# Kernel tuning notes

Measured on AMD Instinct MI355X. Metric: run time of the kernel, lower is better.

Reference implementation:

```python
import jax, jax.numpy as jnp
import numpy as np

NUM_HEADS = 12
SCALE = 1.0 / np.sqrt(768 // NUM_HEADS)  # 0.125


def setup_inputs() -> dict:
    key = jax.random.key(0)
    k1, k2, k3, k4, k5 = jax.random.split(key, 5)
    B, N, C = 4, 2048, 768
    x = jax.random.normal(k1, (B, N, C), dtype=jnp.float32)
    qkv_w = jax.random.normal(k2, (3 * C, C), dtype=jnp.float32) * 0.02
    qkv_b = jax.random.normal(k3, (3 * C,), dtype=jnp.float32) * 0.02
    proj_w = jax.random.normal(k4, (C, C), dtype=jnp.float32) * 0.02
    proj_b = jax.random.normal(k5, (C,), dtype=jnp.float32) * 0.02
    return {"x": x, "qkv_w": qkv_w, "qkv_b": qkv_b, "proj_w": proj_w, "proj_b": proj_b}


def reference(x, qkv_w, qkv_b, proj_w, proj_b):
    B, N, C = x.shape
    H = NUM_HEADS
    Dh = C // H
    # qkv projection (torch Linear: x @ W^T + b)
    qkv = x @ qkv_w.T + qkv_b                      # [B, N, 3C]
    qkv = qkv.reshape(B, N, 3, H, Dh).transpose(2, 0, 3, 1, 4)  # [3, B, H, N, Dh]
    q, k, v = qkv[0], qkv[1], qkv[2]
    q = q * SCALE
    attn = jnp.einsum("bhnd,bhmd->bhnm", q, k)     # [B, H, N, N]
    attn = jax.nn.softmax(attn, axis=-1)
    out = jnp.einsum("bhnm,bhmd->bhnd", attn, v)   # [B, H, N, Dh]
    out = out.transpose(0, 2, 1, 3).reshape(B, N, C)
    out = out @ proj_w.T + proj_b
    return out
```

## Files before the change

### kernel.cpp

```cpp
#include <hip/hip_runtime.h>
#include <math.h>

typedef __attribute__((ext_vector_type(8))) short short8;
typedef __attribute__((ext_vector_type(4))) float f32x4;
typedef __attribute__((ext_vector_type(16))) float f32x16;

namespace {

constexpr int B  = 4;
constexpr int N  = 2048;
constexpr int C  = 768;
constexpr int H  = 12;
constexpr int Dh = 64;
constexpr int M  = B * N;
constexpr int C3 = 3 * C;

constexpr float QSCALE = 0.125f * 1.4426950408889634f;

__device__ inline unsigned short f2bf(float x) {
  unsigned int u = __float_as_uint(x);
  return (unsigned short)((u + 0x7fffu + ((u >> 16) & 1u)) >> 16);
}

__device__ inline unsigned cvt_pk_bf16(float lo, float hi) {
  unsigned r;
  asm("v_cvt_pk_bf16_f32 %0, %1, %2" : "=v"(r) : "v"(lo), "v"(hi));
  return r;
}

__device__ inline void gload_lds16(const void* g, void* lds) {
  __builtin_amdgcn_global_load_lds(
      (const __attribute__((address_space(1))) void*)g,
      (__attribute__((address_space(3))) void*)lds, 16, 0, 0);
}

__device__ inline float max3f(float a, float b, float c) {
  return fmaxf(fmaxf(a, b), c);
}

__global__ __launch_bounds__(256) void cvt_all3(
    const float* __restrict__ x, const float* __restrict__ qw,
    const float* __restrict__ pw, unsigned short* __restrict__ xbf,
    unsigned short* __restrict__ wqkv, unsigned short* __restrict__ wproj) {
  constexpr int n1 = M * C / 4, n2 = C3 * C / 4, n3 = C * C / 4;
  constexpr int tot = n1 + n2 + n3;
  for (int i = blockIdx.x * 256 + threadIdx.x; i < tot; i += gridDim.x * 256) {
    const float4* s; unsigned short* d; int j;
    if (i < n1)            { s = (const float4*)x;  d = xbf;   j = i; }
    else if (i < n1 + n2)  { s = (const float4*)qw; d = wqkv;  j = i - n1; }
    else                   { s = (const float4*)pw; d = wproj; j = i - n1 - n2; }
    float4 v = s[j];
    ushort4 o;
    o.x = f2bf(v.x); o.y = f2bf(v.y); o.z = f2bf(v.z); o.w = f2bf(v.w);
    reinterpret_cast<ushort4*>(d)[j] = o;
  }
}

template <bool QKV_EPI>
__global__ __launch_bounds__(256, 2) void gemm_mfma_bt(
    const unsigned short* __restrict__ A, const unsigned short* __restrict__ Bw,
    const float* __restrict__ bias, void* __restrict__ outp, int Nd, int K) {
  __shared__ alignas(16) unsigned short lA[128 * 64];
  __shared__ alignas(16) unsigned short lB[128 * 64];
  const int t = threadIdx.x, wave = t >> 6, lane = t & 63;
  const int bm = blockIdx.x * 128, bn = blockIdx.y * 128;
  const int wr = (wave >> 1) * 64, wc = (wave & 1) * 64;

  f32x4 acc[4][4];
#pragma unroll
  for (int i = 0; i < 4; ++i)
#pragma unroll
    for (int j = 0; j < 4; ++j) acc[i][j] = (f32x4){0.f, 0.f, 0.f, 0.f};

  const int srow = lane >> 3;
  const int scol = ((lane & 7) ^ srow) * 8;
  const int rb0  = wave * 32;

  for (int k0 = 0; k0 < K; k0 += 64) {
#pragma unroll
    for (int i = 0; i < 4; ++i) {
      const int rb = rb0 + i * 8;
      const unsigned short* ga = A  + (size_t)(bm + rb + srow) * K + k0 + scol;
      const unsigned short* gb = Bw + (size_t)(bn + rb + srow) * K + k0 + scol;
      gload_lds16(ga, (char*)lA + rb * 128);
      gload_lds16(gb, (char*)lB + rb * 128);
    }
    __syncthreads();

#pragma unroll
    for (int kc = 0; kc < 2; ++kc) {
      short8 af[4], bfr[4];
#pragma unroll
      for (int mt = 0; mt < 4; ++mt) {
        const int row = wr + mt * 16 + (lane & 15);
        const int q = (row * 128 + kc * 64 + (lane >> 4) * 16) ^ ((row & 7) << 4);
        af[mt] = *reinterpret_cast<const short8*>((const char*)lA + q);
      }
#pragma unroll
      for (int nt = 0; nt < 4; ++nt) {
        const int row = wc + nt * 16 + (lane & 15);
        const int q = (row * 128 + kc * 64 + (lane >> 4) * 16) ^ ((row & 7) << 4);
        bfr[nt] = *reinterpret_cast<const short8*>((const char*)lB + q);
      }
#pragma unroll
      for (int mt = 0; mt < 4; ++mt)
#pragma unroll
        for (int nt = 0; nt < 4; ++nt)
          acc[mt][nt] = __builtin_amdgcn_mfma_f32_16x16x32_bf16(
              af[mt], bfr[nt], acc[mt][nt], 0, 0, 0);
    }
    __syncthreads();
  }

  const int r0 = (lane >> 4) * 4;
  const int cl = lane & 15;
#pragma unroll
  for (int nt = 0; nt < 4; ++nt) {
    const int col = bn + wc + nt * 16 + cl;
    const float bs = bias[col];
    const float sc = (QKV_EPI && col < C) ? QSCALE : 1.0f;
#pragma unroll
    for (int mt = 0; mt < 4; ++mt) {
#pragma unroll
      for (int r = 0; r < 4; ++r) {
        const size_t row = bm + wr + mt * 16 + r0 + r;
        const float v = acc[mt][nt][r] + bs;
        if (QKV_EPI)
          ((unsigned short*)outp)[row * Nd + col] = f2bf(v * sc);
        else
          ((float*)outp)[row * Nd + col] = v;
      }
    }
  }
}

__global__ __launch_bounds__(256) void vt_prepass(
    const unsigned short* __restrict__ qkvbf, unsigned short* __restrict__ vt) {
  const int bh = blockIdx.x, b = bh / H, h = bh % H;
  const int nt = blockIdx.y;
  __shared__ unsigned short tile[64][72];
  const int t = threadIdx.x;
  const int r = t >> 2, ch = (t & 3) * 16;

  const unsigned short* src =
      qkvbf + (size_t)(b * N + nt * 64 + r) * C3 + 2 * C + h * Dh + ch;
  *reinterpret_cast<int4*>(&tile[r][ch])     = *reinterpret_cast<const int4*>(src);
  *reinterpret_cast<int4*>(&tile[r][ch + 8]) = *reinterpret_cast<const int4*>(src + 8);
  __syncthreads();

  alignas(16) unsigned short vals[16];
#pragma unroll
  for (int i = 0; i < 16; ++i) vals[i] = tile[ch + i][r];
  unsigned short* dst = vt + ((size_t)bh * Dh + r) * N + nt * 64 + ch;
  *reinterpret_cast<int4*>(dst)     = *reinterpret_cast<int4*>(&vals[0]);
  *reinterpret_cast<int4*>(dst + 8) = *reinterpret_cast<int4*>(&vals[8]);
}

__global__ __launch_bounds__(128, 2) void attn_mfma32(
    const unsigned short* __restrict__ qkvbf,
    const unsigned short* __restrict__ vt,
    unsigned short* __restrict__ ctx) {
  const int bh = blockIdx.x, b = bh / H, h = bh % H;
  const int qt = blockIdx.y;
  const int t = threadIdx.x;
  const int wave = t >> 6, lane = t & 63;
  const int ql = lane & 31;
  const int hi = lane >> 5;
  const int q0 = qt * 128 + wave * 64;

  __shared__ alignas(16) char lds[2][16384];

  short8 qfa[4], qfb[4];
  {
    const unsigned short* qa =
        qkvbf + (size_t)(b * N + q0 + ql) * C3 + h * Dh + 8 * hi;
    const unsigned short* qb = qa + (size_t)32 * C3;
#pragma unroll
    for (int s = 0; s < 4; ++s) {
      int4 va = *reinterpret_cast<const int4*>(qa + 16 * s);
      int4 vb = *reinterpret_cast<const int4*>(qb + 16 * s);
      qfa[s] = *reinterpret_cast<short8*>(&va);
      qfb[s] = *reinterpret_cast<short8*>(&vb);
    }
  }

  f32x16 zz;
#pragma unroll
  for (int r = 0; r < 16; ++r) zz[r] = 0.f;
  f32x16 oa0 = zz, oa1 = zz, ob0 = zz, ob1 = zz;
  float mra = -INFINITY, mrb = -INFINITY, la = 0.f, lb = 0.f;

  const int rl = lane >> 3;
  const int cse = ((lane & 7) ^ rl) * 8;
  const unsigned short* kstg =
      qkvbf + (size_t)(b * N + rl) * C3 + C + h * Dh + cse;
  const unsigned short* vstg = vt + ((size_t)bh * Dh + rl) * N + cse;

  auto stage = [&](int kt, char* buf) {
    if (wave == 0) {
      const unsigned short* kp = kstg + (size_t)(kt * 64) * C3;
#pragma unroll
      for (int j = 0; j < 8; ++j)
        gload_lds16(kp + (size_t)(j * 8) * C3, buf + j * 1024);
    } else {
      const unsigned short* vp = vstg + kt * 64;
#pragma unroll
      for (int j = 0; j < 8; ++j)
        gload_lds16(vp + (size_t)(j * 8) * N, buf + 8192 + j * 1024);
    }
  };

  constexpr int NT = N / 64;

  auto kaddr = [&](int row, int s) {
    return (row * 128 + 32 * s + 16 * hi) ^ ((row & 7) << 4);
  };

  stage(0, lds[0]);
  __syncthreads();

  for (int kt = 0; kt < NT; ++kt) {
    const char* bufc = lds[kt & 1];
    if (kt + 1 < NT) stage(kt + 1, lds[(kt + 1) & 1]);

    short8 k0[4], k1[4];
#pragma unroll
    for (int s = 0; s < 4; ++s) {
      k0[s] = *reinterpret_cast<const short8*>(bufc + kaddr(ql, s));
      k1[s] = *reinterpret_cast<const short8*>(bufc + kaddr(32 + ql, s));
    }

    f32x16 sa0, sa1, sb0, sb1;
    __builtin_amdgcn_s_setprio(1);
    sa0 = __builtin_amdgcn_mfma_f32_32x32x16_bf16(k0[0], qfa[0], zz, 0, 0, 0);
    sa1 = __builtin_amdgcn_mfma_f32_32x32x16_bf16(k1[0], qfa[0], zz, 0, 0, 0);
    sb0 = __builtin_amdgcn_mfma_f32_32x32x16_bf16(k0[0], qfb[0], zz, 0, 0, 0);
    sb1 = __builtin_amdgcn_mfma_f32_32x32x16_bf16(k1[0], qfb[0], zz, 0, 0, 0);
#pragma unroll
    for (int s = 1; s < 4; ++s) {
      sa0 = __builtin_amdgcn_mfma_f32_32x32x16_bf16(k0[s], qfa[s], sa0, 0, 0, 0);
      sa1 = __builtin_amdgcn_mfma_f32_32x32x16_bf16(k1[s], qfa[s], sa1, 0, 0, 0);
      sb0 = __builtin_amdgcn_mfma_f32_32x32x16_bf16(k0[s], qfb[s], sb0, 0, 0, 0);
      sb1 = __builtin_amdgcn_mfma_f32_32x32x16_bf16(k1[s], qfb[s], sb1, 0, 0, 0);
    }
    __builtin_amdgcn_s_setprio(0);

    short8 vfr[8];
    const char* bufv = bufc + 8192;
#pragma unroll
    for (int s = 0; s < 4; ++s) {
      vfr[2 * s]     = *reinterpret_cast<const short8*>(bufv + kaddr(ql, s));
      vfr[2 * s + 1] = *reinterpret_cast<const short8*>(bufv + kaddr(32 + ql, s));
    }

    auto rmax = [&](const f32x16& x, const f32x16& y) {
      float t0 = max3f(x[0], x[1], x[2]);
      float t1 = max3f(x[3], x[4], x[5]);
      float t2 = max3f(x[6], x[7], x[8]);
      float t3 = max3f(x[9], x[10], x[11]);
      float t4 = max3f(x[12], x[13], x[14]);
      float t5 = max3f(x[15], y[0], y[1]);
      float t6 = max3f(y[2], y[3], y[4]);
      float t7 = max3f(y[5], y[6], y[7]);
      float t8 = max3f(y[8], y[9], y[10]);
      float t9 = max3f(y[11], y[12], y[13]);
      float ta = fmaxf(y[14], y[15]);
      t0 = max3f(t0, t1, t2);
      t3 = max3f(t3, t4, t5);
      t6 = max3f(t6, t7, t8);
      t9 = max3f(t9, ta, t0);
      return max3f(t3, t6, t9);
    };
    const float mxa = rmax(sa0, sa1);
    const float mxb = rmax(sb0, sb1);
    const bool fast = (mxa <= mra + 8.f) && (mxb <= mrb + 8.f);
    if (!__all(fast)) {
      const float nma = fmaxf(mra, fmaxf(mxa, __shfl_xor(mxa, 32)));
      const float nmb = fmaxf(mrb, fmaxf(mxb, __shfl_xor(mxb, 32)));
      const float ca = __builtin_amdgcn_exp2f(mra - nma);
      const float cb = __builtin_amdgcn_exp2f(mrb - nmb);
      la *= ca; lb *= cb;
#pragma unroll
      for (int r = 0; r < 16; ++r) {
        const int qr = (r & 3) + 8 * (r >> 2) + 4 * hi;
        const float cra = __shfl(ca, qr);
        const float crb = __shfl(cb, qr);
        oa0[r] *= cra; oa1[r] *= cra;
        ob0[r] *= crb; ob1[r] *= crb;
      }
      mra = nma; mrb = nmb;
    }

    auto mkfrag = [&](const f32x16& sh, float mr, float& lacc,
                      short8& fA, short8& fB) {
      float e[16];
#pragma unroll
      for (int r = 0; r < 16; ++r) e[r] = __builtin_amdgcn_exp2f(sh[r] - mr);
      lacc += (((e[0] + e[1]) + (e[2] + e[3])) + ((e[4] + e[5]) + (e[6] + e[7]))) +
              (((e[8] + e[9]) + (e[10] + e[11])) + ((e[12] + e[13]) + (e[14] + e[15])));
      unsigned w[8];
#pragma unroll
      for (int tt = 0; tt < 4; ++tt) {
        w[2 * tt]     = cvt_pk_bf16(e[4 * tt], e[4 * tt + 1]);
        w[2 * tt + 1] = cvt_pk_bf16(e[4 * tt + 2], e[4 * tt + 3]);
      }
      unsigned a0 = w[0], a1 = w[1], b0 = w[2], b1 = w[3];
      asm("v_permlane32_swap_b32 %0, %1" : "+v"(a0), "+v"(b0));
      asm("v_permlane32_swap_b32 %0, %1" : "+v"(a1), "+v"(b1));
      int4 p0; p0.x = a0; p0.y = a1; p0.z = b0; p0.w = b1;
      fA = *reinterpret_cast<short8*>(&p0);
      unsigned c0 = w[4], c1 = w[5], d0 = w[6], d1 = w[7];
      asm("v_permlane32_swap_b32 %0, %1" : "+v"(c0), "+v"(d0));
      asm("v_permlane32_swap_b32 %0, %1" : "+v"(c1), "+v"(d1));
      int4 p1; p1.x = c0; p1.y = c1; p1.z = d0; p1.w = d1;
      fB = *reinterpret_cast<short8*>(&p1);
    };
    short8 pa0, pa1, pa2, pa3, pb0, pb1, pb2, pb3;
    mkfrag(sa0, mra, la, pa0, pa1);
    mkfrag(sa1, mra, la, pa2, pa3);
    mkfrag(sb0, mrb, lb, pb0, pb1);
    mkfrag(sb1, mrb, lb, pb2, pb3);

    __builtin_amdgcn_s_setprio(1);
    oa0 = __builtin_amdgcn_mfma_f32_32x32x16_bf16(pa0, vfr[0], oa0, 0, 0, 0);
    oa1 = __builtin_amdgcn_mfma_f32_32x32x16_bf16(pa0, vfr[1], oa1, 0, 0, 0);
    ob0 = __builtin_amdgcn_mfma_f32_32x32x16_bf16(pb0, vfr[0], ob0, 0, 0, 0);
    ob1 = __builtin_amdgcn_mfma_f32_32x32x16_bf16(pb0, vfr[1], ob1, 0, 0, 0);
    oa0 = __builtin_amdgcn_mfma_f32_32x32x16_bf16(pa1, vfr[2], oa0, 0, 0, 0);
    oa1 = __builtin_amdgcn_mfma_f32_32x32x16_bf16(pa1, vfr[3], oa1, 0, 0, 0);
    ob0 = __builtin_amdgcn_mfma_f32_32x32x16_bf16(pb1, vfr[2], ob0, 0, 0, 0);
    ob1 = __builtin_amdgcn_mfma_f32_32x32x16_bf16(pb1, vfr[3], ob1, 0, 0, 0);
    oa0 = __builtin_amdgcn_mfma_f32_32x32x16_bf16(pa2, vfr[4], oa0, 0, 0, 0);
    oa1 = __builtin_amdgcn_mfma_f32_32x32x16_bf16(pa2, vfr[5], oa1, 0, 0, 0);
    ob0 = __builtin_amdgcn_mfma_f32_32x32x16_bf16(pb2, vfr[4], ob0, 0, 0, 0);
    ob1 = __builtin_amdgcn_mfma_f32_32x32x16_bf16(pb2, vfr[5], ob1, 0, 0, 0);
    oa0 = __builtin_amdgcn_mfma_f32_32x32x16_bf16(pa3, vfr[6], oa0, 0, 0, 0);
    oa1 = __builtin_amdgcn_mfma_f32_32x32x16_bf16(pa3, vfr[7], oa1, 0, 0, 0);
    ob0 = __builtin_amdgcn_mfma_f32_32x32x16_bf16(pb3, vfr[6], ob0, 0, 0, 0);
    ob1 = __builtin_amdgcn_mfma_f32_32x32x16_bf16(pb3, vfr[7], ob1, 0, 0, 0);
    __builtin_amdgcn_s_setprio(0);

    __syncthreads();
  }

  la += __shfl_xor(la, 32);
  lb += __shfl_xor(lb, 32);
  const float inva = 1.f / la;
  const float invb = 1.f / lb;
#pragma unroll
  for (int r = 0; r < 16; ++r) {
    const int qr = (r & 3) + 8 * (r >> 2) + 4 * hi;
    const float ira = __shfl(inva, qr);
    const float irb = __shfl(invb, qr);
    unsigned short* rowa = ctx + (size_t)(b * N + q0 + qr) * C + h * Dh;
    unsigned short* rowb = rowa + (size_t)32 * C;
    rowa[ql]      = f2bf(oa0[r] * ira);
    rowa[32 + ql] = f2bf(oa1[r] * ira);
    rowb[ql]      = f2bf(ob0[r] * irb);
    rowb[32 + ql] = f2bf(ob1[r] * irb);
  }
}

}

extern "C" void kernel_launch(void* const* d_in, const int* in_sizes, int n_in,
                              void* d_out, int out_size, void* d_ws, size_t ws_size,
                              hipStream_t stream) {
  const float* x      = (const float*)d_in[0];
  const float* qkv_w  = (const float*)d_in[1];
  const float* qkv_b  = (const float*)d_in[2];
  const float* proj_w = (const float*)d_in[3];
  const float* proj_b = (const float*)d_in[4];
  float* out = (float*)d_out;

  unsigned short* qkvbf = (unsigned short*)d_ws;
  unsigned short* ctx   = qkvbf + (size_t)M * C3;
  unsigned short* vt    = ctx + (size_t)M * C;
  unsigned short* xbf   = vt + (size_t)M * C;
  unsigned short* wqkv  = xbf + (size_t)M * C;
  unsigned short* wproj = wqkv + (size_t)C3 * C;

  cvt_all3<<<2048, 256, 0, stream>>>(x, qkv_w, proj_w, xbf, wqkv, wproj);

  gemm_mfma_bt<true>
      <<<dim3(M / 128, C3 / 128), 256, 0, stream>>>(xbf, wqkv, qkv_b, qkvbf, C3, C);
  vt_prepass<<<dim3(B * H, N / 64), 256, 0, stream>>>(qkvbf, vt);
  attn_mfma32<<<dim3(B * H, N / 128), 128, 0, stream>>>(qkvbf, vt, ctx);
  gemm_mfma_bt<false>
      <<<dim3(M / 128, C / 128), 256, 0, stream>>>(ctx, wproj, proj_b, out, C, C);
}
```

Measured before the change: 148.4 us.

## Split attention KV range in two and merge partial softmax results

Splits the flash-attention key/value loop into two halves run by separate blocks (grid z=2). Each block writes its unnormalized partial output in bf16 along with the running max and sum, and a new merge kernel combines them with log-sum-exp rescaling. The goal is to double the block count so more of the GPU's compute units are busy, since the original grid of 768 two-wave blocks may underfill the device. The cost is extra global traffic for the partials, an extra kernel launch, and some precision loss from storing unnormalized bf16 partials; part0 reuses the xbf buffer.

```diff
diff --git a/kernel.cpp b/kernel.cpp
--- a/kernel.cpp
+++ b/kernel.cpp
@@ -20,6 +20,10 @@
 __device__ inline unsigned short f2bf(float x) {
   unsigned int u = __float_as_uint(x);
   return (unsigned short)((u + 0x7fffu + ((u >> 16) & 1u)) >> 16);
+}
+
+__device__ inline float bf2f(unsigned short x) {
+  return __uint_as_float((unsigned)x << 16);
 }
 
 __device__ inline unsigned cvt_pk_bf16(float lo, float hi) {
@@ -159,9 +163,15 @@
 __global__ __launch_bounds__(128, 2) void attn_mfma32(
     const unsigned short* __restrict__ qkvbf,
     const unsigned short* __restrict__ vt,
-    unsigned short* __restrict__ ctx) {
+    unsigned short* __restrict__ part0, unsigned short* __restrict__ part1,
+    float2* __restrict__ ml0, float2* __restrict__ ml1) {
   const int bh = blockIdx.x, b = bh / H, h = bh % H;
   const int qt = blockIdx.y;
+  const int z  = blockIdx.z;
+  const int kv0 = z * (N / 2);
+  unsigned short* part = z ? part1 : part0;
+  float2* mlp = z ? ml1 : ml0;
+
   const int t = threadIdx.x;
   const int wave = t >> 6, lane = t & 63;
   const int ql = lane & 31;
@@ -193,8 +203,8 @@
   const int rl = lane >> 3;
   const int cse = ((lane & 7) ^ rl) * 8;
   const unsigned short* kstg =
-      qkvbf + (size_t)(b * N + rl) * C3 + C + h * Dh + cse;
-  const unsigned short* vstg = vt + ((size_t)bh * Dh + rl) * N + cse;
+      qkvbf + (size_t)(b * N + kv0 + rl) * C3 + C + h * Dh + cse;
+  const unsigned short* vstg = vt + ((size_t)bh * Dh + rl) * N + kv0 + cse;
 
   auto stage = [&](int kt, char* buf) {
     if (wave == 0) {
@@ -210,7 +220,7 @@
     }
   };
 
-  constexpr int NT = N / 64;
+  constexpr int NT = N / 2 / 64;
 
   auto kaddr = [&](int row, int s) {
     return (row * 128 + 32 * s + 16 * hi) ^ ((row & 7) << 4);
@@ -345,20 +355,52 @@
 
   la += __shfl_xor(la, 32);
   lb += __shfl_xor(lb, 32);
-  const float inva = 1.f / la;
-  const float invb = 1.f / lb;
+  if (hi == 0) {
+    mlp[(size_t)bh * N + q0 + ql]      = make_float2(mra, la);
+    mlp[(size_t)bh * N + q0 + 32 + ql] = make_float2(mrb, lb);
+  }
 #pragma unroll
   for (int r = 0; r < 16; ++r) {
     const int qr = (r & 3) + 8 * (r >> 2) + 4 * hi;
-    const float ira = __shfl(inva, qr);
-    const float irb = __shfl(invb, qr);
-    unsigned short* rowa = ctx + (size_t)(b * N + q0 + qr) * C + h * Dh;
+    unsigned short* rowa = part + (size_t)(b * N + q0 + qr) * C + h * Dh;
     unsigned short* rowb = rowa + (size_t)32 * C;
-    rowa[ql]      = f2bf(oa0[r] * ira);
-    rowa[32 + ql] = f2bf(oa1[r] * ira);
-    rowb[ql]      = f2bf(ob0[r] * irb);
-    rowb[32 + ql] = f2bf(ob1[r] * irb);
-  }
+    rowa[ql]      = f2bf(oa0[r]);
+    rowa[32 + ql] = f2bf(oa1[r]);
+    rowb[ql]      = f2bf(ob0[r]);
+    rowb[32 + ql] = f2bf(ob1[r]);
+  }
+}
+
+__global__ __launch_bounds__(256) void merge_splits(
+    const unsigned short* __restrict__ p0, const unsigned short* __restrict__ p1,
+    const float2* __restrict__ ml0, const float2* __restrict__ ml1,
+    unsigned short* __restrict__ ctx) {
+  const int idx = blockIdx.x * 256 + threadIdx.x;
+  const int r = idx / 96, c = (idx % 96) * 8;
+  const int b = r >> 11, n = r & 2047, h = c >> 6;
+  const size_t mli = (size_t)(b * H + h) * N + n;
+  const float2 u = ml0[mli], v = ml1[mli];
+  const float m  = fmaxf(u.x, v.x);
+  const float c0 = __builtin_amdgcn_exp2f(u.x - m);
+  const float c1 = __builtin_amdgcn_exp2f(v.x - m);
+  const float inv = 1.f / (u.y * c0 + v.y * c1);
+  const float s0 = c0 * inv, s1 = c1 * inv;
+  const size_t off = (size_t)r * C + c;
+  int4 a = *reinterpret_cast<const int4*>(p0 + off);
+  int4 bb = *reinterpret_cast<const int4*>(p1 + off);
+  short8 x0 = *reinterpret_cast<short8*>(&a);
+  short8 x1 = *reinterpret_cast<short8*>(&bb);
+  unsigned w[4];
+#pragma unroll
+  for (int j = 0; j < 4; ++j) {
+    float f0 = bf2f((unsigned short)x0[2 * j]) * s0 +
+               bf2f((unsigned short)x1[2 * j]) * s1;
+    float f1 = bf2f((unsigned short)x0[2 * j + 1]) * s0 +
+               bf2f((unsigned short)x1[2 * j + 1]) * s1;
+    w[j] = cvt_pk_bf16(f0, f1);
+  }
+  int4 o; o.x = w[0]; o.y = w[1]; o.z = w[2]; o.w = w[3];
+  *reinterpret_cast<int4*>(ctx + off) = o;
 }
 
 }
@@ -379,13 +421,19 @@
   unsigned short* xbf   = vt + (size_t)M * C;
   unsigned short* wqkv  = xbf + (size_t)M * C;
   unsigned short* wproj = wqkv + (size_t)C3 * C;
+  unsigned short* part1 = wproj + (size_t)C * C;
+  float2* ml0 = (float2*)(part1 + (size_t)M * C);
+  float2* ml1 = ml0 + (size_t)B * H * N;
+  unsigned short* part0 = xbf;
 
   cvt_all3<<<2048, 256, 0, stream>>>(x, qkv_w, proj_w, xbf, wqkv, wproj);
 
   gemm_mfma_bt<true>
       <<<dim3(M / 128, C3 / 128), 256, 0, stream>>>(xbf, wqkv, qkv_b, qkvbf, C3, C);
   vt_prepass<<<dim3(B * H, N / 64), 256, 0, stream>>>(qkvbf, vt);
-  attn_mfma32<<<dim3(B * H, N / 128), 128, 0, stream>>>(qkvbf, vt, ctx);
+  attn_mfma32<<<dim3(B * H, N / 128, 2), 128, 0, stream>>>(
+      qkvbf, vt, part0, part1, ml0, ml1);
+  merge_splits<<<M * 96 / 256, 256, 0, stream>>>(part0, part1, ml0, ml1, ctx);
   gemm_mfma_bt<false>
       <<<dim3(M / 128, C / 128), 256, 0, stream>>>(ctx, wproj, proj_b, out, C, C);
 }
```

Measured after the change: 159.6 us. 1.08x slower.

## Software-pipeline attention: overlap next QK^T with softmax and PV, triple-buffer LDS

Applied to the files above, without the earlier changes.

The attention kernel is restructured so the QK^T MFMAs for the next key tile are issued before the softmax and PV of the current tile, using two ping-ponged score register sets and a three-deep LDS ring with explicit vmcnt waits. The row-sum is now computed on the matrix cores by multiplying P with a ones fragment, which removes the VALU adds and the final cross-lane shuffles. The goal is to hide exp/VALU latency behind MFMA work and to cut barrier stalls. The costs are higher register pressure from the extra score and l accumulators, the dropped occupancy hint of 2 blocks, and 48KB of LDS per block.

```diff
diff --git a/kernel.cpp b/kernel.cpp
--- a/kernel.cpp
+++ b/kernel.cpp
@@ -36,6 +36,61 @@
 
 __device__ inline float max3f(float a, float b, float c) {
   return fmaxf(fmaxf(a, b), c);
+}
+
+__device__ __forceinline__ float rmax2(const f32x16& x, const f32x16& y) {
+  float t0 = max3f(x[0], x[1], x[2]);
+  float t1 = max3f(x[3], x[4], x[5]);
+  float t2 = max3f(x[6], x[7], x[8]);
+  float t3 = max3f(x[9], x[10], x[11]);
+  float t4 = max3f(x[12], x[13], x[14]);
+  float t5 = max3f(x[15], y[0], y[1]);
+  float t6 = max3f(y[2], y[3], y[4]);
+  float t7 = max3f(y[5], y[6], y[7]);
+  float t8 = max3f(y[8], y[9], y[10]);
+  float t9 = max3f(y[11], y[12], y[13]);
+  float ta = fmaxf(y[14], y[15]);
+  t0 = max3f(t0, t1, t2);
+  t3 = max3f(t3, t4, t5);
+  t6 = max3f(t6, t7, t8);
+  t9 = max3f(t9, ta, t0);
+  return max3f(t3, t6, t9);
+}
+
+__device__ __forceinline__ void mkfrag(const f32x16& sh, float mr,
+                                       short8& fA, short8& fB) {
+  float e[16];
+#pragma unroll
+  for (int r = 0; r < 16; ++r) e[r] = __builtin_amdgcn_exp2f(sh[r] - mr);
+  unsigned w[8];
+#pragma unroll
+  for (int tt = 0; tt < 4; ++tt) {
+    w[2 * tt]     = cvt_pk_bf16(e[4 * tt], e[4 * tt + 1]);
+    w[2 * tt + 1] = cvt_pk_bf16(e[4 * tt + 2], e[4 * tt + 3]);
+  }
+  unsigned a0 = w[0], a1 = w[1], b0 = w[2], b1 = w[3];
+  asm("v_permlane32_swap_b32 %0, %1" : "+v"(a0), "+v"(b0));
+  asm("v_permlane32_swap_b32 %0, %1" : "+v"(a1), "+v"(b1));
+  int4 p0; p0.x = (int)a0; p0.y = (int)a1; p0.z = (int)b0; p0.w = (int)b1;
+  fA = *reinterpret_cast<short8*>(&p0);
+  unsigned c0 = w[4], c1 = w[5], d0 = w[6], d1 = w[7];
+  asm("v_permlane32_swap_b32 %0, %1" : "+v"(c0), "+v"(d0));
+  asm("v_permlane32_swap_b32 %0, %1" : "+v"(c1), "+v"(d1));
+  int4 p1; p1.x = (int)c0; p1.y = (int)c1; p1.z = (int)d0; p1.w = (int)d1;
+  fB = *reinterpret_cast<short8*>(&p1);
+}
+
+__device__ __forceinline__ void rescaleO(
+    f32x16& oa0, f32x16& oa1, f32x16& ob0, f32x16& ob1,
+    f32x16& la, f32x16& lb, float ca, float cb, int hi) {
+#pragma unroll
+  for (int r = 0; r < 16; ++r) {
+    const int qr = (r & 3) + 8 * (r >> 2) + 4 * hi;
+    const float cra = __shfl(ca, qr);
+    const float crb = __shfl(cb, qr);
+    oa0[r] *= cra; oa1[r] *= cra; la[r] *= cra;
+    ob0[r] *= crb; ob1[r] *= crb; lb[r] *= crb;
+  }
 }
 
 __global__ __launch_bounds__(256) void cvt_all3(
@@ -156,7 +211,92 @@
   *reinterpret_cast<int4*>(dst + 8) = *reinterpret_cast<int4*>(&vals[8]);
 }
 
-__global__ __launch_bounds__(128, 2) void attn_mfma32(
+#define QK_ACC4(SA0, SA1, SB0, SB1, K0, K1, S)                                 \
+  SA0 = __builtin_amdgcn_mfma_f32_32x32x16_bf16(K0, qfa[S], SA0, 0, 0, 0);     \
+  SA1 = __builtin_amdgcn_mfma_f32_32x32x16_bf16(K1, qfa[S], SA1, 0, 0, 0);     \
+  SB0 = __builtin_amdgcn_mfma_f32_32x32x16_bf16(K0, qfb[S], SB0, 0, 0, 0);     \
+  SB1 = __builtin_amdgcn_mfma_f32_32x32x16_bf16(K1, qfb[S], SB1, 0, 0, 0);
+
+#define ATTN_STEP(T, SA0C, SA1C, SB0C, SB1C, SA0N, SA1N, SB0N, SB1N)           \
+  {                                                                            \
+    const int T_ = (T);                                                        \
+    if (T_ + 1 < NT) {                                                         \
+      asm volatile("s_waitcnt vmcnt(0)" ::: "memory");                         \
+      __builtin_amdgcn_s_barrier();                                            \
+      if (T_ + 2 < NT) stage(T_ + 2);                                          \
+      const char* bn_ = lds[(T_ + 1) % 3];                                     \
+      short8 ka_ = *reinterpret_cast<const short8*>(bn_ + kaddr(ql, 0));       \
+      short8 kb_ = *reinterpret_cast<const short8*>(bn_ + kaddr(32 + ql, 0));  \
+      __builtin_amdgcn_s_setprio(1);                                           \
+      SA0N = __builtin_amdgcn_mfma_f32_32x32x16_bf16(ka_, qfa[0], zz, 0, 0, 0);\
+      SA1N = __builtin_amdgcn_mfma_f32_32x32x16_bf16(kb_, qfa[0], zz, 0, 0, 0);\
+      SB0N = __builtin_amdgcn_mfma_f32_32x32x16_bf16(ka_, qfb[0], zz, 0, 0, 0);\
+      SB1N = __builtin_amdgcn_mfma_f32_32x32x16_bf16(kb_, qfb[0], zz, 0, 0, 0);\
+      ka_ = *reinterpret_cast<const short8*>(bn_ + kaddr(ql, 1));              \
+      kb_ = *reinterpret_cast<const short8*>(bn_ + kaddr(32 + ql, 1));         \
+      QK_ACC4(SA0N, SA1N, SB0N, SB1N, ka_, kb_, 1)                             \
+      ka_ = *reinterpret_cast<const short8*>(bn_ + kaddr(ql, 2));              \
+      kb_ = *reinterpret_cast<const short8*>(bn_ + kaddr(32 + ql, 2));         \
+      QK_ACC4(SA0N, SA1N, SB0N, SB1N, ka_, kb_, 2)                             \
+      ka_ = *reinterpret_cast<const short8*>(bn_ + kaddr(ql, 3));              \
+      kb_ = *reinterpret_cast<const short8*>(bn_ + kaddr(32 + ql, 3));         \
+      QK_ACC4(SA0N, SA1N, SB0N, SB1N, ka_, kb_, 3)                             \
+      __builtin_amdgcn_s_setprio(0);                                           \
+    }                                                                          \
+    const char* bc_ = lds[T_ % 3];                                             \
+    const char* bv_ = bc_ + 8192;                                              \
+    short8 vf0_ = *reinterpret_cast<const short8*>(bv_ + kaddr(ql, 0));        \
+    short8 vf1_ = *reinterpret_cast<const short8*>(bv_ + kaddr(32 + ql, 0));   \
+    short8 vf2_ = *reinterpret_cast<const short8*>(bv_ + kaddr(ql, 1));        \
+    short8 vf3_ = *reinterpret_cast<const short8*>(bv_ + kaddr(32 + ql, 1));   \
+    short8 vf4_ = *reinterpret_cast<const short8*>(bv_ + kaddr(ql, 2));        \
+    short8 vf5_ = *reinterpret_cast<const short8*>(bv_ + kaddr(32 + ql, 2));   \
+    short8 vf6_ = *reinterpret_cast<const short8*>(bv_ + kaddr(ql, 3));        \
+    short8 vf7_ = *reinterpret_cast<const short8*>(bv_ + kaddr(32 + ql, 3));   \
+    const float mxa_ = rmax2(SA0C, SA1C);                                      \
+    const float mxb_ = rmax2(SB0C, SB1C);                                      \
+    if (!__all((mxa_ <= mra + 8.f) && (mxb_ <= mrb + 8.f))) {                  \
+      const float nma_ = fmaxf(mra, fmaxf(mxa_, __shfl_xor(mxa_, 32)));        \
+      const float nmb_ = fmaxf(mrb, fmaxf(mxb_, __shfl_xor(mxb_, 32)));        \
+      const float ca_ = __builtin_amdgcn_exp2f(mra - nma_);                    \
+      const float cb_ = __builtin_amdgcn_exp2f(mrb - nmb_);                    \
+      rescaleO(oa0, oa1, ob0, ob1, l_a, l_b, ca_, cb_, hi);                    \
+      mra = nma_; mrb = nmb_;                                                  \
+    }                                                                          \
+    short8 pa0_, pa1_, pa2_, pa3_, pb0_, pb1_, pb2_, pb3_;                     \
+    mkfrag(SA0C, mra, pa0_, pa1_);                                             \
+    mkfrag(SA1C, mra, pa2_, pa3_);                                             \
+    mkfrag(SB0C, mrb, pb0_, pb1_);                                             \
+    mkfrag(SB1C, mrb, pb2_, pb3_);                                             \
+    __builtin_amdgcn_s_setprio(1);                                             \
+    l_a = __builtin_amdgcn_mfma_f32_32x32x16_bf16(pa0_, ones, l_a, 0, 0, 0);   \
+    l_b = __builtin_amdgcn_mfma_f32_32x32x16_bf16(pb0_, ones, l_b, 0, 0, 0);   \
+    oa0 = __builtin_amdgcn_mfma_f32_32x32x16_bf16(pa0_, vf0_, oa0, 0, 0, 0);   \
+    oa1 = __builtin_amdgcn_mfma_f32_32x32x16_bf16(pa0_, vf1_, oa1, 0, 0, 0);   \
+    ob0 = __builtin_amdgcn_mfma_f32_32x32x16_bf16(pb0_, vf0_, ob0, 0, 0, 0);   \
+    ob1 = __builtin_amdgcn_mfma_f32_32x32x16_bf16(pb0_, vf1_, ob1, 0, 0, 0);   \
+    l_a = __builtin_amdgcn_mfma_f32_32x32x16_bf16(pa1_, ones, l_a, 0, 0, 0);   \
+    l_b = __builtin_amdgcn_mfma_f32_32x32x16_bf16(pb1_, ones, l_b, 0, 0, 0);   \
+    oa0 = __builtin_amdgcn_mfma_f32_32x32x16_bf16(pa1_, vf2_, oa0, 0, 0, 0);   \
+    oa1 = __builtin_amdgcn_mfma_f32_32x32x16_bf16(pa1_, vf3_, oa1, 0, 0, 0);   \
+    ob0 = __builtin_amdgcn_mfma_f32_32x32x16_bf16(pb1_, vf2_, ob0, 0, 0, 0);   \
+    ob1 = __builtin_amdgcn_mfma_f32_32x32x16_bf16(pb1_, vf3_, ob1, 0, 0, 0);   \
+    l_a = __builtin_amdgcn_mfma_f32_32x32x16_bf16(pa2_, ones, l_a, 0, 0, 0);   \
+    l_b = __builtin_amdgcn_mfma_f32_32x32x16_bf16(pb2_, ones, l_b, 0, 0, 0);   \
+    oa0 = __builtin_amdgcn_mfma_f32_32x32x16_bf16(pa2_, vf4_, oa0, 0, 0, 0);   \
+    oa1 = __builtin_amdgcn_mfma_f32_32x32x16_bf16(pa2_, vf5_, oa1, 0, 0, 0);   \
+    ob0 = __builtin_amdgcn_mfma_f32_32x32x16_bf16(pb2_, vf4_, ob0, 0, 0, 0);   \
+    ob1 = __builtin_amdgcn_mfma_f32_32x32x16_bf16(pb2_, vf5_, ob1, 0, 0, 0);   \
+    l_a = __builtin_amdgcn_mfma_f32_32x32x16_bf16(pa3_, ones, l_a, 0, 0, 0);   \
+    l_b = __builtin_amdgcn_mfma_f32_32x32x16_bf16(pb3_, ones, l_b, 0, 0, 0);   \
+    oa0 = __builtin_amdgcn_mfma_f32_32x32x16_bf16(pa3_, vf6_, oa0, 0, 0, 0);   \
+    oa1 = __builtin_amdgcn_mfma_f32_32x32x16_bf16(pa3_, vf7_, oa1, 0, 0, 0);   \
+    ob0 = __builtin_amdgcn_mfma_f32_32x32x16_bf16(pb3_, vf6_, ob0, 0, 0, 0);   \
+    ob1 = __builtin_amdgcn_mfma_f32_32x32x16_bf16(pb3_, vf7_, ob1, 0, 0, 0);   \
+    __builtin_amdgcn_s_setprio(0);                                             \
+  }
+
+__global__ __launch_bounds__(128) void attn_pipe(
     const unsigned short* __restrict__ qkvbf,
     const unsigned short* __restrict__ vt,
     unsigned short* __restrict__ ctx) {
@@ -164,11 +304,10 @@
   const int qt = blockIdx.y;
   const int t = threadIdx.x;
   const int wave = t >> 6, lane = t & 63;
-  const int ql = lane & 31;
-  const int hi = lane >> 5;
+  const int ql = lane & 31, hi = lane >> 5;
   const int q0 = qt * 128 + wave * 64;
 
-  __shared__ alignas(16) char lds[2][16384];
+  __shared__ alignas(16) char lds[3][16384];
 
   short8 qfa[4], qfb[4];
   {
@@ -187,8 +326,12 @@
   f32x16 zz;
 #pragma unroll
   for (int r = 0; r < 16; ++r) zz[r] = 0.f;
-  f32x16 oa0 = zz, oa1 = zz, ob0 = zz, ob1 = zz;
-  float mra = -INFINITY, mrb = -INFINITY, la = 0.f, lb = 0.f;
+  f32x16 oa0 = zz, oa1 = zz, ob0 = zz, ob1 = zz, l_a = zz, l_b = zz;
+  float mra = -INFINITY, mrb = -INFINITY;
+
+  short8 ones;
+#pragma unroll
+  for (int i = 0; i < 8; ++i) ones[i] = (short)0x3F80;
 
   const int rl = lane >> 3;
   const int cse = ((lane & 7) ^ rl) * 8;
@@ -196,17 +339,18 @@
       qkvbf + (size_t)(b * N + rl) * C3 + C + h * Dh + cse;
   const unsigned short* vstg = vt + ((size_t)bh * Dh + rl) * N + cse;
 
-  auto stage = [&](int kt, char* buf) {
+  auto stage = [&](int j) {
+    char* buf = lds[j % 3];
     if (wave == 0) {
-      const unsigned short* kp = kstg + (size_t)(kt * 64) * C3;
-#pragma unroll
-      for (int j = 0; j < 8; ++j)
-        gload_lds16(kp + (size_t)(j * 8) * C3, buf + j * 1024);
+      const unsigned short* kp = kstg + (size_t)(j * 64) * C3;
+#pragma unroll
+      for (int i = 0; i < 8; ++i)
+        gload_lds16(kp + (size_t)(i * 8) * C3, buf + i * 1024);
     } else {
-      const unsigned short* vp = vstg + kt * 64;
-#pragma unroll
-      for (int j = 0; j < 8; ++j)
-        gload_lds16(vp + (size_t)(j * 8) * N, buf + 8192 + j * 1024);
+      const unsigned short* vp = vstg + j * 64;
+#pragma unroll
+      for (int i = 0; i < 8; ++i)
+        gload_lds16(vp + (size_t)(i * 8) * N, buf + 8192 + i * 1024);
     }
   };
 
@@ -216,142 +360,41 @@
     return (row * 128 + 32 * s + 16 * hi) ^ ((row & 7) << 4);
   };
 
-  stage(0, lds[0]);
-  __syncthreads();
-
-  for (int kt = 0; kt < NT; ++kt) {
-    const char* bufc = lds[kt & 1];
-    if (kt + 1 < NT) stage(kt + 1, lds[(kt + 1) & 1]);
-
-    short8 k0[4], k1[4];
-#pragma unroll
-    for (int s = 0; s < 4; ++s) {
-      k0[s] = *reinterpret_cast<const short8*>(bufc + kaddr(ql, s));
-      k1[s] = *reinterpret_cast<const short8*>(bufc + kaddr(32 + ql, s));
-    }
-
-    f32x16 sa0, sa1, sb0, sb1;
-    __builtin_amdgcn_s_setprio(1);
-    sa0 = __builtin_amdgcn_mfma_f32_32x32x16_bf16(k0[0], qfa[0], zz, 0, 0, 0);
-    sa1 = __builtin_amdgcn_mfma_f32_32x32x16_bf16(k1[0], qfa[0], zz, 0, 0, 0);
-    sb0 = __builtin_amdgcn_mfma_f32_32x32x16_bf16(k0[0], qfb[0], zz, 0, 0, 0);
-    sb1 = __builtin_amdgcn_mfma_f32_32x32x16_bf16(k1[0], qfb[0], zz, 0, 0, 0);
+  stage(0);
+  stage(1);
+  asm volatile("s_waitcnt vmcnt(8)" ::: "memory");
+  __builtin_amdgcn_s_barrier();
+
+  f32x16 xa0, xa1, xb0, xb1, ya0, ya1, yb0, yb1;
+  {
+    const char* b0 = lds[0];
+    short8 ka = *reinterpret_cast<const short8*>(b0 + kaddr(ql, 0));
+    short8 kb = *reinterpret_cast<const short8*>(b0 + kaddr(32 + ql, 0));
+    xa0 = __builtin_amdgcn_mfma_f32_32x32x16_bf16(ka, qfa[0], zz, 0, 0, 0);
+    xa1 = __builtin_amdgcn_mfma_f32_32x32x16_bf16(kb, qfa[0], zz, 0, 0, 0);
+    xb0 = __builtin_amdgcn_mfma_f32_32x32x16_bf16(ka, qfb[0], zz, 0, 0, 0);
+    xb1 = __builtin_amdgcn_mfma_f32_32x32x16_bf16(kb, qfb[0], zz, 0, 0, 0);
 #pragma unroll
     for (int s = 1; s < 4; ++s) {
-      sa0 = __builtin_amdgcn_mfma_f32_32x32x16_bf16(k0[s], qfa[s], sa0, 0, 0, 0);
-      sa1 = __builtin_amdgcn_mfma_f32_32x32x16_bf16(k1[s], qfa[s], sa1, 0, 0, 0);
-      sb0 = __builtin_amdgcn_mfma_f32_32x32x16_bf16(k0[s], qfb[s], sb0, 0, 0, 0);
-      sb1 = __builtin_amdgcn_mfma_f32_32x32x16_bf16(k1[s], qfb[s], sb1, 0, 0, 0);
-    }
-    __builtin_amdgcn_s_setprio(0);
-
-    short8 vfr[8];
-    const char* bufv = bufc + 8192;
-#pragma unroll
-    for (int s = 0; s < 4; ++s) {
-      vfr[2 * s]     = *reinterpret_cast<const short8*>(bufv + kaddr(ql, s));
-      vfr[2 * s + 1] = *reinterpret_cast<const short8*>(bufv + kaddr(32 + ql, s));
-    }
-
-    auto rmax = [&](const f32x16& x, const f32x16& y) {
-      float t0 = max3f(x[0], x[1], x[2]);
-      float t1 = max3f(x[3], x[4], x[5]);
-      float t2 = max3f(x[6], x[7], x[8]);
-      float t3 = max3f(x[9], x[10], x[11]);
-      float t4 = max3f(x[12], x[13], x[14]);
-      float t5 = max3f(x[15], y[0], y[1]);
-      float t6 = max3f(y[2], y[3], y[4]);
-      float t7 = max3f(y[5], y[6], y[7]);
-      float t8 = max3f(y[8], y[9], y[10]);
-      float t9 = max3f(y[11], y[12], y[13]);
-      float ta = fmaxf(y[14], y[15]);
-      t0 = max3f(t0, t1, t2);
-      t3 = max3f(t3, t4, t5);
-      t6 = max3f(t6, t7, t8);
-      t9 = max3f(t9, ta, t0);
-      return max3f(t3, t6, t9);
-    };
-    const float mxa = rmax(sa0, sa1);
-    const float mxb = rmax(sb0, sb1);
-    const bool fast = (mxa <= mra + 8.f) && (mxb <= mrb + 8.f);
-    if (!__all(fast)) {
-      const float nma = fmaxf(mra, fmaxf(mxa, __shfl_xor(mxa, 32)));
-      const float nmb = fmaxf(mrb, fmaxf(mxb, __shfl_xor(mxb, 32)));
-      const float ca = __builtin_amdgcn_exp2f(mra - nma);
-      const float cb = __builtin_amdgcn_exp2f(mrb - nmb);
-      la *= ca; lb *= cb;
-#pragma unroll
-      for (int r = 0; r < 16; ++r) {
-        const int qr = (r & 3) + 8 * (r >> 2) + 4 * hi;
-        const float cra = __shfl(ca, qr);
-        const float crb = __shfl(cb, qr);
-        oa0[r] *= cra; oa1[r] *= cra;
-        ob0[r] *= crb; ob1[r] *= crb;
-      }
-      mra = nma; mrb = nmb;
-    }
-
-    auto mkfrag = [&](const f32x16& sh, float mr, float& lacc,
-                      short8& fA, short8& fB) {
-      float e[16];
-#pragma unroll
-      for (int r = 0; r < 16; ++r) e[r] = __builtin_amdgcn_exp2f(sh[r] - mr);
-      lacc += (((e[0] + e[1]) + (e[2] + e[3])) + ((e[4] + e[5]) + (e[6] + e[7]))) +
-              (((e[8] + e[9]) + (e[10] + e[11])) + ((e[12] + e[13]) + (e[14] + e[15])));
-      unsigned w[8];
-#pragma unroll
-      for (int tt = 0; tt < 4; ++tt) {
-        w[2 * tt]     = cvt_pk_bf16(e[4 * tt], e[4 * tt + 1]);
-        w[2 * tt + 1] = cvt_pk_bf16(e[4 * tt + 2], e[4 * tt + 3]);
-      }
-      unsigned a0 = w[0], a1 = w[1], b0 = w[2], b1 = w[3];
-      asm("v_permlane32_swap_b32 %0, %1" : "+v"(a0), "+v"(b0));
-      asm("v_permlane32_swap_b32 %0, %1" : "+v"(a1), "+v"(b1));
-      int4 p0; p0.x = a0; p0.y = a1; p0.z = b0; p0.w = b1;
-      fA = *reinterpret_cast<short8*>(&p0);
-      unsigned c0 = w[4], c1 = w[5], d0 = w[6], d1 = w[7];
-      asm("v_permlane32_swap_b32 %0, %1" : "+v"(c0), "+v"(d0));
-      asm("v_permlane32_swap_b32 %0, %1" : "+v"(c1), "+v"(d1));
-      int4 p1; p1.x = c0; p1.y = c1; p1.z = d0; p1.w = d1;
-      fB = *reinterpret_cast<short8*>(&p1);
-    };
-    short8 pa0, pa1, pa2, pa3, pb0, pb1, pb2, pb3;
-    mkfrag(sa0, mra, la, pa0, pa1);
-    mkfrag(sa1, mra, la, pa2, pa3);
-    mkfrag(sb0, mrb, lb, pb0, pb1);
-    mkfrag(sb1, mrb, lb, pb2, pb3);
-
-    __builtin_amdgcn_s_setprio(1);
-    oa0 = __builtin_amdgcn_mfma_f32_32x32x16_bf16(pa0, vfr[0], oa0, 0, 0, 0);
-    oa1 = __builtin_amdgcn_mfma_f32_32x32x16_bf16(pa0, vfr[1], oa1, 0, 0, 0);
-    ob0 = __builtin_amdgcn_mfma_f32_32x32x16_bf16(pb0, vfr[0], ob0, 0, 0, 0);
-    ob1 = __builtin_amdgcn_mfma_f32_32x32x16_bf16(pb0, vfr[1], ob1, 0, 0, 0);
-    oa0 = __builtin_amdgcn_mfma_f32_32x32x16_bf16(pa1, vfr[2], oa0, 0, 0, 0);
-    oa1 = __builtin_amdgcn_mfma_f32_32x32x16_bf16(pa1, vfr[3], oa1, 0, 0, 0);
-    ob0 = __builtin_amdgcn_mfma_f32_32x32x16_bf16(pb1, vfr[2], ob0, 0, 0, 0);
-    ob1 = __builtin_amdgcn_mfma_f32_32x32x16_bf16(pb1, vfr[3], ob1, 0, 0, 0);
-    oa0 = __builtin_amdgcn_mfma_f32_32x32x16_bf16(pa2, vfr[4], oa0, 0, 0, 0);
-    oa1 = __builtin_amdgcn_mfma_f32_32x32x16_bf16(pa2, vfr[5], oa1, 0, 0, 0);
-    ob0 = __builtin_amdgcn_mfma_f32_32x32x16_bf16(pb2, vfr[4], ob0, 0, 0, 0);
-    ob1 = __builtin_amdgcn_mfma_f32_32x32x16_bf16(pb2, vfr[5], ob1, 0, 0, 0);
-    oa0 = __builtin_amdgcn_mfma_f32_32x32x16_bf16(pa3, vfr[6], oa0, 0, 0, 0);
-    oa1 = __builtin_amdgcn_mfma_f32_32x32x16_bf16(pa3, vfr[7], oa1, 0, 0, 0);
-    ob0 = __builtin_amdgcn_mfma_f32_32x32x16_bf16(pb3, vfr[6], ob0, 0, 0, 0);
-    ob1 = __builtin_amdgcn_mfma_f32_32x32x16_bf16(pb3, vfr[7], ob1, 0, 0, 0);
-    __builtin_amdgcn_s_setprio(0);
-
-    __syncthreads();
-  }
-
-  la += __shfl_xor(la, 32);
-  lb += __shfl_xor(lb, 32);
-  const float inva = 1.f / la;
-  const float invb = 1.f / lb;
+      ka = *reinterpret_cast<const short8*>(b0 + kaddr(ql, s));
+      kb = *reinterpret_cast<const short8*>(b0 + kaddr(32 + ql, s));
+      xa0 = __builtin_amdgcn_mfma_f32_32x32x16_bf16(ka, qfa[s], xa0, 0, 0, 0);
+      xa1 = __builtin_amdgcn_mfma_f32_32x32x16_bf16(kb, qfa[s], xa1, 0, 0, 0);
+      xb0 = __builtin_amdgcn_mfma_f32_32x32x16_bf16(ka, qfb[s], xb0, 0, 0, 0);
+      xb1 = __builtin_amdgcn_mfma_f32_32x32x16_bf16(kb, qfb[s], xb1, 0, 0, 0);
+    }
+  }
+
+  for (int tp = 0; tp < NT; tp += 2) {
+    ATTN_STEP(tp,     xa0, xa1, xb0, xb1, ya0, ya1, yb0, yb1)
+    ATTN_STEP(tp + 1, ya0, ya1, yb0, yb1, xa0, xa1, xb0, xb1)
+  }
+
 #pragma unroll
   for (int r = 0; r < 16; ++r) {
     const int qr = (r & 3) + 8 * (r >> 2) + 4 * hi;
-    const float ira = __shfl(inva, qr);
-    const float irb = __shfl(invb, qr);
+    const float ira = 1.f / l_a[r];
+    const float irb = 1.f / l_b[r];
     unsigned short* rowa = ctx + (size_t)(b * N + q0 + qr) * C + h * Dh;
     unsigned short* rowb = rowa + (size_t)32 * C;
     rowa[ql]      = f2bf(oa0[r] * ira);
@@ -385,7 +428,7 @@
   gemm_mfma_bt<true>
       <<<dim3(M / 128, C3 / 128), 256, 0, stream>>>(xbf, wqkv, qkv_b, qkvbf, C3, C);
   vt_prepass<<<dim3(B * H, N / 64), 256, 0, stream>>>(qkvbf, vt);
-  attn_mfma32<<<dim3(B * H, N / 128), 128, 0, stream>>>(qkvbf, vt, ctx);
+  attn_pipe<<<dim3(B * H, N / 128), 128, 0, stream>>>(qkvbf, vt, ctx);
   gemm_mfma_bt<false>
       <<<dim3(M / 128, C / 128), 256, 0, stream>>>(ctx, wproj, proj_b, out, C, C);
 }
```

Result: slower. 207.8 us (+40.0%).
